# Kernel optimization log

Hardware: AMD Instinct MI355X
Metric: run time of the kernel (lower is better)

The kernel has to match this reference:

```python
import math
import jax, jax.numpy as jnp
import numpy as np

R = 6  # number of Hermite functions
EPS = 1e-5  # BatchNorm eps


def setup_inputs() -> dict:
    key = jax.random.key(0)
    k1, k2 = jax.random.split(key)
    B, C, H, W = 8, 64, 128, 128
    out_c = 64
    x = jax.random.normal(k1, (B, C, H, W), dtype=jnp.float32)
    gamma = jnp.ones((C,), dtype=jnp.float32)
    beta = jnp.zeros((C,), dtype=jnp.float32)
    Wt = jax.random.normal(k2, (out_c, C), dtype=jnp.float32) * (1.0 / math.sqrt(C))
    b = jnp.zeros((out_c,), dtype=jnp.float32)
    return {"x": x, "gamma": gamma, "beta": beta, "Wt": Wt, "b": b}


def _hermite_funcs(x):
    # x: (B, C, N) -> psi: (B, C, R, N)
    t = jnp.tanh(x) * math.sqrt(2 * R + 1)
    g = jnp.exp(-t * t / 2)
    pi_q = math.pi ** (-0.25)
    p_prev = pi_q * g                      # psi_0
    p_cur = math.sqrt(2.0) * pi_q * t * g  # psi_1
    ps = [p_prev, p_cur]
    for k in range(2, R):  # tiny fixed loop over recurrence order
        p_next = math.sqrt(2.0 / k) * t * p_cur - math.sqrt((k - 1) / k) * p_prev
        ps.append(p_next)
        p_prev, p_cur = p_cur, p_next
    return jnp.stack(ps, axis=2)


def reference(x, gamma, beta, Wt, b):
    B, C, H, W = x.shape
    xf = x.reshape(B, C, H * W)
    # BatchNorm1d (training-mode batch statistics, biased variance)
    mean = jnp.mean(xf, axis=(0, 2), keepdims=True)
    var = jnp.mean((xf - mean) ** 2, axis=(0, 2), keepdims=True)
    xn = (xf - mean) / jnp.sqrt(var + EPS) * gamma[None, :, None] + beta[None, :, None]
    psi = _hermite_funcs(xn)  # (B, C, R, N)
    cost = jnp.einsum('bikd,bid->bik', psi, xn)
    w = jax.nn.softmax(cost, axis=2)
    y = jnp.einsum('bik,bikd->bid', w, psi)  # (B, C, N)
    out = jnp.einsum('oc,bcd->bod', Wt, y) + b[None, :, None]  # 1x1 conv
    return out.reshape(B, Wt.shape[0], H, W)
```

## Files before the change

### kernel.cpp

```cpp
#include <hip/hip_runtime.h>

typedef short short8 __attribute__((ext_vector_type(8)));
typedef float f32x4 __attribute__((ext_vector_type(4)));

#define NB 8
#define NC 64
#define NN 16384
#define NO 64
#define SQRT13 3.605551275463989f


__device__ __forceinline__ unsigned short f2bf(float f) {
    unsigned int u = __builtin_bit_cast(unsigned int, f);
    u += 0x7fffu + ((u >> 16) & 1u);
    return (unsigned short)(u >> 16);
}

__device__ __forceinline__ unsigned int pack_bf2(float lo, float hi) {
    return (unsigned int)f2bf(lo) | ((unsigned int)f2bf(hi) << 16);
}

__device__ __forceinline__ float tanh13(float x) {
    float e = __expf(2.0f * x);
    float r = __builtin_amdgcn_rcpf(e + 1.0f);
    return fmaf(-2.0f * SQRT13, r, SQRT13);
}

__device__ __forceinline__ float yeval(float xv, float a, float bb,
                                       float c0, float c1, float c2,
                                       float c3, float c4, float c5) {
    float t = tanh13(fmaf(xv, a, bb));
    float gg = __expf(-0.5f * t * t);
    float p = c5;
    p = fmaf(p, t, c4);
    p = fmaf(p, t, c3);
    p = fmaf(p, t, c2);
    p = fmaf(p, t, c1);
    p = fmaf(p, t, c0);
    return gg * p;
}

__global__ __launch_bounds__(256) void k_stats(const float* __restrict__ x,
                                               float* __restrict__ part,
                                               const float* __restrict__ Wt,
                                               unsigned short* __restrict__ WtB) {
    int bc = blockIdx.x;
    const float* xp = x + (size_t)bc * NN;
    int tid = threadIdx.x;
    float s = 0.f, ss = 0.f;
    #pragma unroll
    for (int i = 0; i < 16; ++i) {
        float4 v = *(const float4*)(xp + i * 1024 + tid * 4);
        s  += v.x + v.y + v.z + v.w;
        ss += v.x * v.x + v.y * v.y + v.z * v.z + v.w * v.w;
    }
    for (int off = 32; off; off >>= 1) {
        s  += __shfl_down(s, off);
        ss += __shfl_down(ss, off);
    }
    __shared__ float red[2][4];
    int lane = tid & 63, wid = tid >> 6;
    if (lane == 0) { red[0][wid] = s; red[1][wid] = ss; }
    __syncthreads();
    if (tid == 0) {
        part[bc * 2 + 0] = red[0][0] + red[0][1] + red[0][2] + red[0][3];
        part[bc * 2 + 1] = red[1][0] + red[1][1] + red[1][2] + red[1][3];
    }
    if (bc == 0)
        for (int i = tid; i < 4096; i += 256) WtB[i] = f2bf(Wt[i]);
}

__global__ __launch_bounds__(256) void k_cost(const float* __restrict__ x,
                                              const float* __restrict__ part,
                                              const float* __restrict__ gamma,
                                              const float* __restrict__ beta,
                                              float* __restrict__ pp) {
    int bc = blockIdx.x;
    int c  = bc & 63;
    int tid = threadIdx.x;

    float s = 0.f, ss = 0.f;
    #pragma unroll
    for (int bb = 0; bb < NB; ++bb) {
        s  += part[(bb * NC + c) * 2 + 0];
        ss += part[(bb * NC + c) * 2 + 1];
    }
    const float inv = 1.0f / (float)(NB * NN);
    float mean = s * inv;
    float var  = ss * inv - mean * mean;
    float istd = 1.0f / sqrtf(var + 1e-5f);
    float a   = gamma[c] * istd;
    float bsh = beta[c] - mean * a;

    const float* xp = x + (size_t)bc * NN;
    float m[6] = {0.f, 0.f, 0.f, 0.f, 0.f, 0.f};

    #pragma unroll
    for (int half = 0; half < 2; ++half) {
        float4 v[8];
        #pragma unroll
        for (int i = 0; i < 8; ++i)
            v[i] = *(const float4*)(xp + (half * 8 + i) * 1024 + tid * 4);
        #pragma unroll
        for (int i = 0; i < 8; ++i) {
            float xs[4] = {v[i].x, v[i].y, v[i].z, v[i].w};
            #pragma unroll
            for (int j = 0; j < 4; ++j) {
                float xn = fmaf(xs[j], a, bsh);
                float t  = tanh13(xn);
                float g  = __expf(-0.5f * t * t);
                float u  = g * xn;
                m[0] += u;
                u *= t; m[1] += u;
                u *= t; m[2] += u;
                u *= t; m[3] += u;
                u *= t; m[4] += u;
                u *= t; m[5] += u;
            }
        }
    }

    __shared__ float red6[6][4];
    int lane = tid & 63, wid = tid >> 6;
    #pragma unroll
    for (int k = 0; k < 6; ++k) {
        float v = m[k];
        for (int off = 32; off; off >>= 1) v += __shfl_down(v, off);
        if (lane == 0) red6[k][wid] = v;
    }
    __syncthreads();
    if (tid == 0) {
        float M[6];
        #pragma unroll
        for (int k = 0; k < 6; ++k)
            M[k] = red6[k][0] + red6[k][1] + red6[k][2] + red6[k][3];

        float h[6][6];
        #pragma unroll
        for (int k = 0; k < 6; ++k)
            #pragma unroll
            for (int j = 0; j < 6; ++j) h[k][j] = 0.f;
        h[0][0] = 0.7511255444649425f;
        h[1][1] = 1.0622519320271969f;
        for (int k = 2; k < 6; ++k) {
            float s2 = sqrtf(2.0f / k), s1 = sqrtf((k - 1.0f) / k);
            for (int j = 5; j >= 0; --j) {
                float v = (j > 0) ? s2 * h[k - 1][j - 1] : 0.f;
                h[k][j] = v - s1 * h[k - 2][j];
            }
        }
        float cst[6], mx = -1e30f;
        #pragma unroll
        for (int k = 0; k < 6; ++k) {
            float v = 0.f;
            #pragma unroll
            for (int j = 0; j < 6; ++j) v += h[k][j] * M[j];
            cst[k] = v;
            mx = fmaxf(mx, v);
        }
        float sum = 0.f, w[6];
        #pragma unroll
        for (int k = 0; k < 6; ++k) { w[k] = expf(cst[k] - mx); sum += w[k]; }
        float r = 1.0f / sum;
        float* P = pp + (size_t)bc * 8;
        P[0] = a; P[1] = bsh;
        #pragma unroll
        for (int j = 0; j < 6; ++j) {
            float v = 0.f;
            #pragma unroll
            for (int k = 0; k < 6; ++k) v += w[k] * r * h[k][j];
            P[2 + j] = v;
        }
    }
}

__global__ __launch_bounds__(256) void k_out(const float* __restrict__ x,
                                             const unsigned short* __restrict__ WtB,
                                             const float* __restrict__ bias,
                                             const float* __restrict__ pp,
                                             float* __restrict__ out) {
    __shared__ float ppl[512];
    int tid  = threadIdx.x;
    int w    = tid >> 6;
    int l    = tid & 63;
    int grp  = l >> 4;
    int ln   = l & 15;
    int b    = blockIdx.x >> 6;
    int tile = blockIdx.x & 63;

    #pragma unroll
    for (int i0 = 0; i0 < 2; ++i0) {
        int i = i0 * 256 + tid;
        ppl[(i & 7) * 64 + (i >> 3)] = pp[(size_t)b * 512 + i];
    }
    __syncthreads();

    short8 af[2][4];
    #pragma unroll
    for (int kk = 0; kk < 2; ++kk)
        #pragma unroll
        for (int mo = 0; mo < 4; ++mo)
            af[kk][mo] = *reinterpret_cast<const short8*>(
                WtB + (mo * 16 + ln) * 64 + kk * 32 + grp * 8);

    float4 bias4[4];
    #pragma unroll
    for (int mo = 0; mo < 4; ++mo)
        bias4[mo] = *(const float4*)(bias + mo * 16 + grp * 4);

    f32x4 acc[4][4];
    #pragma unroll
    for (int mo = 0; mo < 4; ++mo)
        #pragma unroll
        for (int nd = 0; nd < 4; ++nd)
            acc[mo][nd] = (f32x4){0.f, 0.f, 0.f, 0.f};

    const float* xb = x + (size_t)b * NC * NN + tile * 256 + w * 64 + ln;

    #pragma unroll
    for (int kk = 0; kk < 2; ++kk) {
        unsigned int bu[4][4];
        #pragma unroll
        for (int q = 0; q < 4; ++q) {
            int c0 = kk * 32 + grp * 8 + 2 * q;
            float A0 = ppl[c0],       A1 = ppl[c0 + 1];
            float B0 = ppl[64 + c0],  B1 = ppl[64 + c0 + 1];
            float p00 = ppl[128 + c0], p01 = ppl[192 + c0], p02 = ppl[256 + c0];
            float p03 = ppl[320 + c0], p04 = ppl[384 + c0], p05 = ppl[448 + c0];
            float p10 = ppl[129 + c0], p11 = ppl[193 + c0], p12 = ppl[257 + c0];
            float p13 = ppl[321 + c0], p14 = ppl[385 + c0], p15 = ppl[449 + c0];
            const float* xc0 = xb + (size_t)c0 * NN;
            const float* xc1 = xc0 + NN;
            #pragma unroll
            for (int nd = 0; nd < 4; ++nd) {
                float y0 = yeval(xc0[nd * 16], A0, B0, p00, p01, p02, p03, p04, p05);
                float y1 = yeval(xc1[nd * 16], A1, B1, p10, p11, p12, p13, p14, p15);
                bu[nd][q] = pack_bf2(y0, y1);
            }
        }
        #pragma unroll
        for (int nd = 0; nd < 4; ++nd) {
            union { unsigned int u[4]; short8 s; } U;
            U.u[0] = bu[nd][0]; U.u[1] = bu[nd][1];
            U.u[2] = bu[nd][2]; U.u[3] = bu[nd][3];
            #pragma unroll
            for (int mo = 0; mo < 4; ++mo)
                acc[mo][nd] = __builtin_amdgcn_mfma_f32_16x16x32_bf16(
                    af[kk][mo], U.s, acc[mo][nd], 0, 0, 0);
        }
    }

    float* ob = out + (size_t)b * NO * NN + tile * 256 + w * 64 + ln;
    #pragma unroll
    for (int mo = 0; mo < 4; ++mo) {
        #pragma unroll
        for (int nd = 0; nd < 4; ++nd) {
            f32x4 v = acc[mo][nd];
            ob[(size_t)(mo * 16 + grp * 4 + 0) * NN + nd * 16] = v[0] + bias4[mo].x;
            ob[(size_t)(mo * 16 + grp * 4 + 1) * NN + nd * 16] = v[1] + bias4[mo].y;
            ob[(size_t)(mo * 16 + grp * 4 + 2) * NN + nd * 16] = v[2] + bias4[mo].z;
            ob[(size_t)(mo * 16 + grp * 4 + 3) * NN + nd * 16] = v[3] + bias4[mo].w;
        }
    }
}

extern "C" void kernel_launch(void* const* d_in, const int* in_sizes, int n_in,
                              void* d_out, int out_size, void* d_ws, size_t ws_size,
                              hipStream_t stream) {
    const float* x     = (const float*)d_in[0];
    const float* gamma = (const float*)d_in[1];
    const float* beta  = (const float*)d_in[2];
    const float* Wt    = (const float*)d_in[3];
    const float* bias  = (const float*)d_in[4];
    float* out = (float*)d_out;
    float* ws  = (float*)d_ws;

    float* part = ws;
    float* pp   = ws + 1024;
    unsigned short* WtB = (unsigned short*)(ws + 5120);

    k_stats<<<dim3(NB * NC), dim3(256), 0, stream>>>(x, part, Wt, WtB);
    k_cost<<<dim3(NB * NC), dim3(256), 0, stream>>>(x, part, gamma, beta, pp);
    k_out<<<dim3(NB * NC), dim3(256), 0, stream>>>(x, WtB, bias, pp, out);
}
```

Before: 35.75 us.

## Fuse stats and cost kernels with per-channel atomic counter barrier

New measurement: 63.96 us. 78.9% more time.

```diff
diff --git a/kernel.cpp b/kernel.cpp
--- a/kernel.cpp
+++ b/kernel.cpp
@@ -40,93 +40,92 @@
     return gg * p;
 }
 
-__global__ __launch_bounds__(256) void k_stats(const float* __restrict__ x,
-                                               float* __restrict__ part,
-                                               const float* __restrict__ Wt,
-                                               unsigned short* __restrict__ WtB) {
+__global__ __launch_bounds__(256) void k_sc(const float* __restrict__ x,
+                                            const float* __restrict__ gamma,
+                                            const float* __restrict__ beta,
+                                            const float* __restrict__ Wt,
+                                            float* __restrict__ part,
+                                            int* __restrict__ cnt,
+                                            float* __restrict__ pp,
+                                            unsigned short* __restrict__ WtB) {
     int bc = blockIdx.x;
+    int c  = bc & 63;
+    int tid = threadIdx.x;
+    int lane = tid & 63, wid = tid >> 6;
+
     const float* xp = x + (size_t)bc * NN;
-    int tid = threadIdx.x;
+    float4 v[16];
+    #pragma unroll
+    for (int i = 0; i < 16; ++i)
+        v[i] = *(const float4*)(xp + i * 1024 + tid * 4);
+
     float s = 0.f, ss = 0.f;
     #pragma unroll
     for (int i = 0; i < 16; ++i) {
-        float4 v = *(const float4*)(xp + i * 1024 + tid * 4);
-        s  += v.x + v.y + v.z + v.w;
-        ss += v.x * v.x + v.y * v.y + v.z * v.z + v.w * v.w;
+        s  += v[i].x + v[i].y + v[i].z + v[i].w;
+        ss += v[i].x * v[i].x + v[i].y * v[i].y + v[i].z * v[i].z + v[i].w * v[i].w;
     }
     for (int off = 32; off; off >>= 1) {
         s  += __shfl_down(s, off);
         ss += __shfl_down(ss, off);
     }
-    __shared__ float red[2][4];
-    int lane = tid & 63, wid = tid >> 6;
-    if (lane == 0) { red[0][wid] = s; red[1][wid] = ss; }
+    __shared__ float red2[2][4];
+    if (lane == 0) { red2[0][wid] = s; red2[1][wid] = ss; }
     __syncthreads();
     if (tid == 0) {
-        part[bc * 2 + 0] = red[0][0] + red[0][1] + red[0][2] + red[0][3];
-        part[bc * 2 + 1] = red[1][0] + red[1][1] + red[1][2] + red[1][3];
-    }
+        float ps = red2[0][0] + red2[0][1] + red2[0][2] + red2[0][3];
+        float pq = red2[1][0] + red2[1][1] + red2[1][2] + red2[1][3];
+        __hip_atomic_store(&part[bc * 2 + 0], ps, __ATOMIC_RELAXED, __HIP_MEMORY_SCOPE_AGENT);
+        __hip_atomic_store(&part[bc * 2 + 1], pq, __ATOMIC_RELAXED, __HIP_MEMORY_SCOPE_AGENT);
+        __hip_atomic_fetch_add(&cnt[c], 1, __ATOMIC_RELEASE, __HIP_MEMORY_SCOPE_AGENT);
+    }
+
     if (bc == 0)
         for (int i = tid; i < 4096; i += 256) WtB[i] = f2bf(Wt[i]);
-}
-
-__global__ __launch_bounds__(256) void k_cost(const float* __restrict__ x,
-                                              const float* __restrict__ part,
-                                              const float* __restrict__ gamma,
-                                              const float* __restrict__ beta,
-                                              float* __restrict__ pp) {
-    int bc = blockIdx.x;
-    int c  = bc & 63;
-    int tid = threadIdx.x;
-
-    float s = 0.f, ss = 0.f;
+
+    if (tid == 0) {
+        while (__hip_atomic_load(&cnt[c], __ATOMIC_ACQUIRE, __HIP_MEMORY_SCOPE_AGENT) < NB)
+            __builtin_amdgcn_s_sleep(1);
+    }
+    __syncthreads();
+
+    float cs = 0.f, cq = 0.f;
     #pragma unroll
     for (int bb = 0; bb < NB; ++bb) {
-        s  += part[(bb * NC + c) * 2 + 0];
-        ss += part[(bb * NC + c) * 2 + 1];
+        cs += __hip_atomic_load(&part[(bb * NC + c) * 2 + 0], __ATOMIC_RELAXED, __HIP_MEMORY_SCOPE_AGENT);
+        cq += __hip_atomic_load(&part[(bb * NC + c) * 2 + 1], __ATOMIC_RELAXED, __HIP_MEMORY_SCOPE_AGENT);
     }
     const float inv = 1.0f / (float)(NB * NN);
-    float mean = s * inv;
-    float var  = ss * inv - mean * mean;
+    float mean = cs * inv;
+    float var  = cq * inv - mean * mean;
     float istd = 1.0f / sqrtf(var + 1e-5f);
     float a   = gamma[c] * istd;
     float bsh = beta[c] - mean * a;
 
-    const float* xp = x + (size_t)bc * NN;
     float m[6] = {0.f, 0.f, 0.f, 0.f, 0.f, 0.f};
-
-    #pragma unroll
-    for (int half = 0; half < 2; ++half) {
-        float4 v[8];
-        #pragma unroll
-        for (int i = 0; i < 8; ++i)
-            v[i] = *(const float4*)(xp + (half * 8 + i) * 1024 + tid * 4);
-        #pragma unroll
-        for (int i = 0; i < 8; ++i) {
-            float xs[4] = {v[i].x, v[i].y, v[i].z, v[i].w};
-            #pragma unroll
-            for (int j = 0; j < 4; ++j) {
-                float xn = fmaf(xs[j], a, bsh);
-                float t  = tanh13(xn);
-                float g  = __expf(-0.5f * t * t);
-                float u  = g * xn;
-                m[0] += u;
-                u *= t; m[1] += u;
-                u *= t; m[2] += u;
-                u *= t; m[3] += u;
-                u *= t; m[4] += u;
-                u *= t; m[5] += u;
-            }
-        }
-    }
-
+    #pragma unroll
+    for (int i = 0; i < 16; ++i) {
+        float xs[4] = {v[i].x, v[i].y, v[i].z, v[i].w};
+        #pragma unroll
+        for (int j = 0; j < 4; ++j) {
+            float xn = fmaf(xs[j], a, bsh);
+            float t  = tanh13(xn);
+            float g  = __expf(-0.5f * t * t);
+            float u  = g * xn;
+            m[0] += u;
+            u *= t; m[1] += u;
+            u *= t; m[2] += u;
+            u *= t; m[3] += u;
+            u *= t; m[4] += u;
+            u *= t; m[5] += u;
+        }
+    }
     __shared__ float red6[6][4];
-    int lane = tid & 63, wid = tid >> 6;
     #pragma unroll
     for (int k = 0; k < 6; ++k) {
-        float v = m[k];
-        for (int off = 32; off; off >>= 1) v += __shfl_down(v, off);
-        if (lane == 0) red6[k][wid] = v;
+        float vv = m[k];
+        for (int off = 32; off; off >>= 1) vv += __shfl_down(vv, off);
+        if (lane == 0) red6[k][wid] = vv;
     }
     __syncthreads();
     if (tid == 0) {
@@ -145,18 +144,18 @@
         for (int k = 2; k < 6; ++k) {
             float s2 = sqrtf(2.0f / k), s1 = sqrtf((k - 1.0f) / k);
             for (int j = 5; j >= 0; --j) {
-                float v = (j > 0) ? s2 * h[k - 1][j - 1] : 0.f;
-                h[k][j] = v - s1 * h[k - 2][j];
+                float vv = (j > 0) ? s2 * h[k - 1][j - 1] : 0.f;
+                h[k][j] = vv - s1 * h[k - 2][j];
             }
         }
         float cst[6], mx = -1e30f;
         #pragma unroll
         for (int k = 0; k < 6; ++k) {
-            float v = 0.f;
-            #pragma unroll
-            for (int j = 0; j < 6; ++j) v += h[k][j] * M[j];
-            cst[k] = v;
-            mx = fmaxf(mx, v);
+            float vv = 0.f;
+            #pragma unroll
+            for (int j = 0; j < 6; ++j) vv += h[k][j] * M[j];
+            cst[k] = vv;
+            mx = fmaxf(mx, vv);
         }
         float sum = 0.f, w[6];
         #pragma unroll
@@ -166,10 +165,10 @@
         P[0] = a; P[1] = bsh;
         #pragma unroll
         for (int j = 0; j < 6; ++j) {
-            float v = 0.f;
-            #pragma unroll
-            for (int k = 0; k < 6; ++k) v += w[k] * r * h[k][j];
-            P[2 + j] = v;
+            float vv = 0.f;
+            #pragma unroll
+            for (int k = 0; k < 6; ++k) vv += w[k] * r * h[k][j];
+            P[2 + j] = vv;
         }
     }
 }
@@ -273,13 +272,14 @@
     const float* Wt    = (const float*)d_in[3];
     const float* bias  = (const float*)d_in[4];
     float* out = (float*)d_out;
-    float* ws  = (float*)d_ws;
-
-    float* part = ws;
-    float* pp   = ws + 1024;
-    unsigned short* WtB = (unsigned short*)(ws + 5120);
-
-    k_stats<<<dim3(NB * NC), dim3(256), 0, stream>>>(x, part, Wt, WtB);
-    k_cost<<<dim3(NB * NC), dim3(256), 0, stream>>>(x, part, gamma, beta, pp);
+    float* f   = (float*)d_ws;
+
+    int*   cnt  = (int*)d_ws;
+    float* part = f + 64;
+    float* pp   = f + 1088;
+    unsigned short* WtB = (unsigned short*)(f + 5184);
+
+    hipMemsetAsync(cnt, 0, 64 * sizeof(int), stream);
+    k_sc<<<dim3(NB * NC), dim3(256), 0, stream>>>(x, gamma, beta, Wt, part, cnt, pp, WtB);
     k_out<<<dim3(NB * NC), dim3(256), 0, stream>>>(x, WtB, bias, pp, out);
 }
```
